# Kernel tuning notes

Measured on AMD Instinct MI355X. Metric: run time of the kernel, lower is better.

## Reference

```python
import jax, jax.numpy as jnp
import numpy as np

H, D = 8, 16
F = H * D              # hidden_dim = 128
L = 2                  # num HGT layers
NS = [50000, 20000, 10000]                     # gene, disease, drug node counts
EDGE_META = [(0, 0), (0, 1), (2, 0), (2, 1)]   # (src_type, dst_type) per edge type
ES = [300000, 150000, 100000, 50000]
OFFS = [0, NS[0], NS[0] + NS[1], NS[0] + NS[1] + NS[2]]
NTOT = OFFS[-1]
R, T = len(EDGE_META), len(NS)
SQRT_D = float(np.sqrt(D))


def setup_inputs() -> dict:
    key = jax.random.key(0)
    ks = jax.random.split(key, 32)
    inp = {}
    inp["x_gene"] = jax.random.normal(ks[0], (NS[0], F), jnp.float32)
    inp["x_disease"] = jax.random.normal(ks[1], (NS[1], F), jnp.float32)
    inp["x_drug"] = jax.random.normal(ks[2], (NS[2], F), jnp.float32)
    inp["Wkqv"] = 0.05 * jax.random.normal(ks[3], (L, T, F, 3 * F), jnp.float32)
    inp["bkqv"] = jnp.zeros((L, T, 3 * F), jnp.float32)
    inp["Ak"] = 0.1 * jax.random.normal(ks[4], (L, R, H, D, D), jnp.float32)
    inp["Av"] = 0.1 * jax.random.normal(ks[5], (L, R, H, D, D), jnp.float32)
    inp["prel"] = jnp.ones((L, R, H), jnp.float32)   # PyG inits p_rel to ones
    inp["Wout"] = 0.05 * jax.random.normal(ks[6], (L, T, F, F), jnp.float32)
    inp["bout"] = jnp.zeros((L, T, F), jnp.float32)
    inp["skip"] = jnp.ones((L, T), jnp.float32)      # PyG inits skip to 1
    names = ["ei_gg", "ei_gd", "ei_rg", "ei_rd"]
    for i, (name, (st, dt), E) in enumerate(zip(names, EDGE_META, ES)):
        src = jax.random.randint(ks[10 + 2 * i], (E,), 0, NS[st], dtype=jnp.int32)
        dst = jax.random.randint(ks[11 + 2 * i], (E,), 0, NS[dt], dtype=jnp.int32)
        inp[name] = jnp.stack([src, dst])
    return inp


def _hgt_layer(xs, eis, Wkqv_l, bkqv_l, Ak_l, Av_l, prel_l, Wout_l, bout_l, skip_l):
    """One PyG-style HGTConv layer over the heterogeneous graph."""
    kqv = [x @ Wkqv_l[t] + bkqv_l[t] for t, x in enumerate(xs)]
    k = [a[:, :F].reshape(-1, H, D) for a in kqv]
    q = [a[:, F:2 * F].reshape(-1, H, D) for a in kqv]
    v = [a[:, 2 * F:].reshape(-1, H, D) for a in kqv]

    alphas, dsts, ves = [], [], []
    for r, (st, dt) in enumerate(EDGE_META):
        src, dst = eis[r][0], eis[r][1]
        # relation-specific per-head transforms applied on source node set
        k_r = jnp.einsum('nhd,hde->nhe', k[st], Ak_l[r])
        v_r = jnp.einsum('nhd,hde->nhe', v[st], Av_l[r])
        ke = k_r[src]                      # [E, H, D]
        ve = v_r[src]                      # [E, H, D]
        qe = q[dt][dst]                    # [E, H, D]
        a = (qe * ke).sum(-1) * prel_l[r] / SQRT_D   # [E, H]
        alphas.append(a)
        dsts.append(dst + OFFS[dt])
        ves.append(ve)
    alpha = jnp.concatenate(alphas, 0)     # [Etot, H]
    dstg = jnp.concatenate(dsts, 0)        # [Etot]
    ve = jnp.concatenate(ves, 0)           # [Etot, H, D]

    # segment softmax over all incoming edges per destination node
    amax = jax.ops.segment_max(alpha, dstg, num_segments=NTOT)
    ex = jnp.exp(alpha - amax[dstg])
    denom = jax.ops.segment_sum(ex, dstg, num_segments=NTOT)
    w = ex / denom[dstg]
    out = jax.ops.segment_sum(ve * w[..., None], dstg, num_segments=NTOT)
    out = out.reshape(NTOT, F)

    new_xs = []
    for t, x in enumerate(xs):
        o_t = out[OFFS[t]:OFFS[t + 1]]
        o = jax.nn.gelu(o_t, approximate=False) @ Wout_l[t] + bout_l[t]
        a_s = jax.nn.sigmoid(skip_l[t])
        new_xs.append(a_s * o + (1.0 - a_s) * x)
    return new_xs


def reference(x_gene, x_disease, x_drug, Wkqv, bkqv, Ak, Av, prel, Wout, bout,
              skip, ei_gg, ei_gd, ei_rg, ei_rd):
    xs = [x_gene, x_disease, x_drug]
    eis = [ei_gg, ei_gd, ei_rg, ei_rd]
    for l in range(L):
        new = _hgt_layer(xs, eis, Wkqv[l], bkqv[l], Ak[l], Av[l], prel[l],
                         Wout[l], bout[l], skip[l])
        # encoder: dropout(relu(conv_out)) + residual; dropout = identity (eval)
        xs = [jax.nn.relu(n) + x for n, x in zip(new, xs)]
    return tuple(xs)
```

## Files before the change

kernel.cpp:

```cpp
#include <hip/hip_runtime.h>


#define NTOT  80000
#define ETOT  600000
#define NSRC  120000
#define SLOTS 128

typedef unsigned short u16;
typedef unsigned int   u32;
typedef __attribute__((ext_vector_type(8))) short short8;
typedef __attribute__((ext_vector_type(4))) float f32x4;

__device__ __forceinline__ float bf2f(u16 u){
  union { u32 i; float f; } v; v.i = ((u32)u) << 16; return v.f;
}
__device__ __forceinline__ u16 f2bf(float f){
  union { float f; u32 i; } v; v.f = f;
  u32 x = v.i;
  return (u16)((x + 0x7fffu + ((x >> 16) & 1u)) >> 16);
}
__device__ __forceinline__ void unp4(uint4 a, float* o){
  union { u32 i; float f; } t;
  t.i = a.x << 16;        o[0]=t.f;  t.i = a.x & 0xffff0000u; o[1]=t.f;
  t.i = a.y << 16;        o[2]=t.f;  t.i = a.y & 0xffff0000u; o[3]=t.f;
  t.i = a.z << 16;        o[4]=t.f;  t.i = a.z & 0xffff0000u; o[5]=t.f;
  t.i = a.w << 16;        o[6]=t.f;  t.i = a.w & 0xffff0000u; o[7]=t.f;
}
__device__ __forceinline__ void load16bf(const u16* p, float* o){
  unp4(*(const uint4*)p, o); unp4(*(const uint4*)(p + 8), o + 8);
}


#define PR0 2560000
#define PR1 (PR0 + NTOT)
#define PR2 (PR1 + 8*32768)
#define PR3 (PR2 + 2*6*16384)
#define PR4 (PR3 + 2048)

__global__ __launch_bounds__(256) void prep_all(
    const float* __restrict__ xg, const float* __restrict__ xd,
    const float* __restrict__ xr, float* __restrict__ X, u16* __restrict__ Xbf,
    int* __restrict__ cnt,
    const float* __restrict__ Wkqv, const float* __restrict__ bkqv,
    const float* __restrict__ Ak, const float* __restrict__ Av,
    const float* __restrict__ Wout,
    u16* __restrict__ WeffT, u16* __restrict__ WqT, u16* __restrict__ WoutT,
    float* __restrict__ beff)
{
  int i = blockIdx.x * 256 + threadIdx.x;
  if (i < PR0){
    const float* src; int off;
    if (i < 1600000)      { src = xg; off = i; }
    else if (i < 2240000) { src = xd; off = i - 1600000; }
    else                  { src = xr; off = i - 2240000; }
    float4 v = ((const float4*)src)[off];
    ((float4*)X)[i] = v;
    uint2 b;
    b.x = (u32)f2bf(v.x) | ((u32)f2bf(v.y) << 16);
    b.y = (u32)f2bf(v.z) | ((u32)f2bf(v.w) << 16);
    ((uint2*)Xbf)[i] = b;
    return;
  }
  if (i < PR1){ cnt[i - PR0] = 0; return; }
  if (i < PR2){
    int j = i - PR1;
    int lr = j >> 15, rem = j & 32767, n = rem >> 7, k = rem & 127;
    int l = lr >> 2, r = lr & 3;
    int st = (r >= 2) ? 2 : 0;
    const float* W = Wkqv + (size_t)(l*3 + st) * 49152;
    float acc = 0.f;
    if (n < 128){
      int h = n >> 4, e = n & 15;
      const float* Am = Ak + (size_t)(l*4 + r) * 2048 + h*256;
#pragma unroll
      for (int d = 0; d < 16; d++) acc += W[k*384 + h*16 + d] * Am[d*16 + e];
    } else {
      int n2 = n - 128, h = n2 >> 4, e = n2 & 15;
      const float* Am = Av + (size_t)(l*4 + r) * 2048 + h*256;
#pragma unroll
      for (int d = 0; d < 16; d++) acc += W[k*384 + 256 + h*16 + d] * Am[d*16 + e];
    }
    WeffT[j] = f2bf(acc);
    return;
  }
  if (i < PR3){
    int j = i - PR2;
    if (j < 6*16384){
      int lt = j >> 14, rem = j & 16383, n = rem >> 7, k = rem & 127;
      WqT[j] = f2bf(Wkqv[(size_t)lt*49152 + k*384 + 128 + n]);
    } else {
      int j2 = j - 6*16384;
      int lt = j2 >> 14, rem = j2 & 16383, n = rem >> 7, k = rem & 127;
      WoutT[j2] = f2bf(Wout[(size_t)lt*16384 + k*128 + n]);
    }
    return;
  }
  if (i < PR4){
    int m = i - PR3;
    int lr = m >> 8, jj = m & 255;
    int l = lr >> 2, r = lr & 3;
    int st = (r >= 2) ? 2 : 0;
    const float* b = bkqv + (size_t)(l*3 + st) * 384;
    float acc = 0.f;
    if (jj < 128){
      int h = jj >> 4, e = jj & 15;
      const float* Am = Ak + (size_t)(l*4 + r) * 2048 + h*256;
#pragma unroll
      for (int d = 0; d < 16; d++) acc += b[h*16 + d] * Am[d*16 + e];
    } else {
      int j2 = jj - 128, h = j2 >> 4, e = j2 & 15;
      const float* Am = Av + (size_t)(l*4 + r) * 2048 + h*256;
#pragma unroll
      for (int d = 0; d < 16; d++) acc += b[256 + h*16 + d] * Am[d*16 + e];
    }
    beff[lr * 256 + jj] = acc;
  }
}


__global__ __launch_bounds__(256) void scatter_direct(
    const int* __restrict__ e0, const int* __restrict__ e1,
    const int* __restrict__ e2, const int* __restrict__ e3,
    int* __restrict__ cnt, int* __restrict__ elist)
{
  int e = blockIdx.x * 256 + threadIdx.x;
  if (e >= ETOT) return;
  const int* ei; int E, loc, offd, rnoff, rel;
  if (e < 300000)      { ei = e0; E = 300000; loc = e;          offd = 0;     rnoff = 0;      rel = 0; }
  else if (e < 450000) { ei = e1; E = 150000; loc = e - 300000; offd = 50000; rnoff = 50000;  rel = 1; }
  else if (e < 550000) { ei = e2; E = 100000; loc = e - 450000; offd = 0;     rnoff = 100000; rel = 2; }
  else                 { ei = e3; E = 50000;  loc = e - 550000; offd = 50000; rnoff = 110000; rel = 3; }
  int src = ei[loc], dst = ei[E + loc];
  int dstg = offd + dst;
  int pos = atomicAdd(&cnt[dstg], 1);
  if (pos < SLOTS) elist[dstg*SLOTS + pos] = ((rnoff + src) << 2) | rel;
}


__device__ __forceinline__ void stage_bt(const u16* __restrict__ src, u16* BTl){
  int tid = threadIdx.x;
  const uint4* g = (const uint4*)src;
  uint4 tmp[8];
#pragma unroll
  for (int i = 0; i < 8; i++) tmp[i] = g[tid + i*256];
#pragma unroll
  for (int i = 0; i < 8; i++){
    int L = (tid + i*256) * 16;
    int Ls = L ^ (((L >> 8) & 7) << 4);
    *(uint4*)((char*)BTl + Ls) = tmp[i];
  }
  __syncthreads();
}

__device__ __forceinline__ void gemm_core16(
    const u16* __restrict__ A, const u16* BTl, int M, int bm,
    f32x4 acc[8])
{
  int tid = threadIdx.x;
  int lane = tid & 63, w = tid >> 6;
  int quad = lane >> 4, lm = lane & 15;
  int row = bm + w*16 + lm;
  short8 af[4];
  if (row < M){
    const u16* ap = A + (size_t)row*128 + quad*8;
#pragma unroll
    for (int c = 0; c < 4; c++) af[c] = *(const short8*)(ap + c*32);
  } else {
    short8 z = {0,0,0,0,0,0,0,0};
#pragma unroll
    for (int c = 0; c < 4; c++) af[c] = z;
  }
#pragma unroll
  for (int nt = 0; nt < 8; nt++) acc[nt] = (f32x4){0.f,0.f,0.f,0.f};
#pragma unroll
  for (int nt = 0; nt < 8; nt++){
    int rowb = nt*16 + lm;
    int base = rowb*256 + quad*16;
    int sw = (rowb & 7) << 4;
#pragma unroll
    for (int c = 0; c < 4; c++){
      short8 bf = *(const short8*)((const char*)BTl + ((base + c*64) ^ sw));
      acc[nt] = __builtin_amdgcn_mfma_f32_16x16x32_bf16(af[c], bf, acc[nt], 0, 0, 0);
    }
  }
}

__global__ __launch_bounds__(256) void mfma_gemm_qkv(
    const u16* __restrict__ Xbf,
    const u16* __restrict__ WqTl, const float* __restrict__ bl,
    const u16* __restrict__ WeffTl, const float* __restrict__ beffl,
    u16* __restrict__ qg, u16* __restrict__ kv)
{
  __shared__ u16 BTl[16384];
  int by = blockIdx.x;
  const u16* A; const u16* BT; const float* bias;
  u16* C; int ldc, bm, M, bn;
  if (by < 1252){
    int t, roff;
    if (by < 782)       { t = 0; bm = by*64;         M = 50000; roff = 0; }
    else if (by < 1095) { t = 1; bm = (by-782)*64;   M = 20000; roff = 50000; }
    else                { t = 2; bm = (by-1095)*64;  M = 10000; roff = 70000; }
    A = Xbf + (size_t)roff*128;
    BT = WqTl + (size_t)t*16384;
    bias = bl + (size_t)t*384 + 128;
    C = qg + (size_t)roff*128; ldc = 128; bn = 0;
  } else {
    int idx = by - 1252;
    bn = (idx < 1878) ? 0 : 128;
    int tile = (idx < 1878) ? idx : idx - 1878;
    int r, soff, ooff;
    if (tile < 782)       { r = 0; bm = tile*64;        M = 50000; soff = 0;     ooff = 0; }
    else if (tile < 1564) { r = 1; bm = (tile-782)*64;  M = 50000; soff = 0;     ooff = 50000; }
    else if (tile < 1721) { r = 2; bm = (tile-1564)*64; M = 10000; soff = 70000; ooff = 100000; }
    else                  { r = 3; bm = (tile-1721)*64; M = 10000; soff = 70000; ooff = 110000; }
    A = Xbf + (size_t)soff*128;
    BT = WeffTl + (size_t)r*32768 + (size_t)bn*128;
    bias = beffl + (size_t)r*256 + bn;
    C = kv + (size_t)ooff*256 + bn; ldc = 256;
  }
  stage_bt(BT, BTl);
  f32x4 acc[8];
  gemm_core16(A, BTl, M, bm, acc);
  int lane = threadIdx.x & 63, w = threadIdx.x >> 6;
  int quad = lane >> 4, lm = lane & 15;
#pragma unroll
  for (int nt = 0; nt < 8; nt++){
    int col = nt*16 + lm;
    float bb = bias[col];
#pragma unroll
    for (int i = 0; i < 4; i++){
      int r = bm + w*16 + quad*4 + i;
      if (r < M) C[(size_t)r*ldc + col] = f2bf(acc[nt][i] + bb);
    }
  }
}

__global__ __launch_bounds__(256) void mfma_gemm_out(
    const u16* __restrict__ Gall, const u16* __restrict__ WoutTl,
    const float* __restrict__ bl, const float* __restrict__ skipl,
    float* __restrict__ Xall, u16* __restrict__ Xbfall)
{
  __shared__ u16 BTl[16384];
  int by = blockIdx.x;
  int t, bm, M, roff;
  if (by < 782)       { t = 0; bm = by*64;         M = 50000; roff = 0; }
  else if (by < 1095) { t = 1; bm = (by-782)*64;   M = 20000; roff = 50000; }
  else                { t = 2; bm = (by-1095)*64;  M = 10000; roff = 70000; }
  stage_bt(WoutTl + (size_t)t*16384, BTl);
  const u16* A = Gall + (size_t)roff*128;
  const float* bias = bl + (size_t)t*128;
  float* X = Xall + (size_t)roff*128;
  u16* Xb = Xbfall ? (Xbfall + (size_t)roff*128) : (u16*)0;
  f32x4 acc[8];
  gemm_core16(A, BTl, M, bm, acc);
  float a_s = 1.f / (1.f + expf(-skipl[t]));
  float b_s = 1.f - a_s;
  int lane = threadIdx.x & 63, w = threadIdx.x >> 6;
  int quad = lane >> 4, lm = lane & 15;
#pragma unroll
  for (int nt = 0; nt < 8; nt++){
    int col = nt*16 + lm;
    float bb = bias[col];
#pragma unroll
    for (int i = 0; i < 4; i++){
      int r = bm + w*16 + quad*4 + i;
      if (r < M){
        float* xp = X + (size_t)r*128 + col;
        float x = *xp;
        float o = acc[nt][i] + bb;
        float xn = fmaxf(a_s*o + b_s*x, 0.f) + x;
        *xp = xn;
        if (Xb) Xb[(size_t)r*128 + col] = f2bf(xn);
      }
    }
  }
}


__global__ __launch_bounds__(256) void attn_kernel(
    u16* __restrict__ qg,
    const u16* __restrict__ kv,
    const float* __restrict__ prel,
    const int* __restrict__ cnt,
    const int* __restrict__ elist)
{
  int gid = blockIdx.x * 256 + threadIdx.x;
  int n = gid >> 4;
  if (n >= NTOT) return;
  int lane = threadIdx.x & 63;
  int sub = (lane >> 3) & 1;
  int h = lane & 7;
  float sc0 = prel[0*8+h]*0.25f, sc1 = prel[1*8+h]*0.25f,
        sc2 = prel[2*8+h]*0.25f, sc3 = prel[3*8+h]*0.25f;
  float q[16];
  load16bf(qg + (size_t)n * 128 + h*16, q);
  float acc[16] = {};
  float dsum = 0.f;
  int start = n * SLOTS, c = cnt[n];
  if (c > SLOTS) c = SLOTS;

  auto edge = [&](int ev, uint4 ka, uint4 kb, uint4 va, uint4 vb){
    float ke[16], ve[16];
    unp4(ka, ke); unp4(kb, ke + 8);
    unp4(va, ve); unp4(vb, ve + 8);
    float a = 0.f;
#pragma unroll
    for (int d = 0; d < 16; d++) a += q[d] * ke[d];
    int r = ev & 3;
    float s = (r == 0) ? sc0 : (r == 1) ? sc1 : (r == 2) ? sc2 : sc3;
    float ex = expf(a * s);
    dsum += ex;
#pragma unroll
    for (int d = 0; d < 16; d++) acc[d] += ex * ve[d];
  };

  int idx = sub;
#pragma unroll 1
  for (; idx + 6 < c; idx += 8){
    int e0 = elist[start + idx + 0], e1 = elist[start + idx + 2],
        e2 = elist[start + idx + 4], e3 = elist[start + idx + 6];
    const u16* p0 = kv + (size_t)(e0 >> 2) * 256 + h*16;
    const u16* p1 = kv + (size_t)(e1 >> 2) * 256 + h*16;
    const u16* p2 = kv + (size_t)(e2 >> 2) * 256 + h*16;
    const u16* p3 = kv + (size_t)(e3 >> 2) * 256 + h*16;
    uint4 k0a = *(const uint4*)p0,         k0b = *(const uint4*)(p0 + 8);
    uint4 k1a = *(const uint4*)p1,         k1b = *(const uint4*)(p1 + 8);
    uint4 k2a = *(const uint4*)p2,         k2b = *(const uint4*)(p2 + 8);
    uint4 k3a = *(const uint4*)p3,         k3b = *(const uint4*)(p3 + 8);
    uint4 v0a = *(const uint4*)(p0 + 128), v0b = *(const uint4*)(p0 + 136);
    uint4 v1a = *(const uint4*)(p1 + 128), v1b = *(const uint4*)(p1 + 136);
    uint4 v2a = *(const uint4*)(p2 + 128), v2b = *(const uint4*)(p2 + 136);
    uint4 v3a = *(const uint4*)(p3 + 128), v3b = *(const uint4*)(p3 + 136);
    edge(e0, k0a, k0b, v0a, v0b);
    edge(e1, k1a, k1b, v1a, v1b);
    edge(e2, k2a, k2b, v2a, v2b);
    edge(e3, k3a, k3b, v3a, v3b);
  }
#pragma unroll 1
  for (; idx < c; idx += 2){
    int ev = elist[start + idx];
    const u16* p = kv + (size_t)(ev >> 2) * 256 + h*16;
    uint4 ka = *(const uint4*)p,         kb = *(const uint4*)(p + 8);
    uint4 va = *(const uint4*)(p + 128), vb = *(const uint4*)(p + 136);
    edge(ev, ka, kb, va, vb);
  }

  dsum += __shfl_xor(dsum, 8);
#pragma unroll
  for (int d = 0; d < 16; d++) acc[d] += __shfl_xor(acc[d], 8);

  if (sub == 0){
    float inv = (c > 0) ? 1.f / dsum : 0.f;
    u16 o[16];
#pragma unroll
    for (int d = 0; d < 16; d++){
      float x = acc[d] * inv;
      o[d] = f2bf(0.5f * x * (1.f + erff(x * 0.70710678118654752f)));
    }
    uint4 p0, p1;
    p0.x = o[0]|(o[1]<<16);   p0.y = o[2]|(o[3]<<16);
    p0.z = o[4]|(o[5]<<16);   p0.w = o[6]|(o[7]<<16);
    p1.x = o[8]|(o[9]<<16);   p1.y = o[10]|(o[11]<<16);
    p1.z = o[12]|(o[13]<<16); p1.w = o[14]|(o[15]<<16);
    u16* op = qg + (size_t)n * 128 + h*16;
    *(uint4*)op = p0; *(uint4*)(op + 8) = p1;
  }
}


extern "C" void kernel_launch(void* const* d_in, const int* in_sizes, int n_in,
                              void* d_out, int out_size, void* d_ws, size_t ws_size,
                              hipStream_t stream)
{
  const float* xg   = (const float*)d_in[0];
  const float* xd   = (const float*)d_in[1];
  const float* xr_  = (const float*)d_in[2];
  const float* Wkqv = (const float*)d_in[3];
  const float* bkqv = (const float*)d_in[4];
  const float* Ak   = (const float*)d_in[5];
  const float* Av   = (const float*)d_in[6];
  const float* prel = (const float*)d_in[7];
  const float* Wout = (const float*)d_in[8];
  const float* bout = (const float*)d_in[9];
  const float* skip = (const float*)d_in[10];
  const int* ei[4] = {(const int*)d_in[11], (const int*)d_in[12],
                      (const int*)d_in[13], (const int*)d_in[14]};

  float* X = (float*)d_out;

  char* p = (char*)d_ws;
  auto alloc = [&](size_t b)->void*{ void* r = (void*)p; p += (b + 255) & ~(size_t)255; return r; };
  int*   cnt   = (int*)  alloc((size_t)NTOT * 4);
  int*   elist = (int*)  alloc((size_t)NTOT * SLOTS * 4);
  float* beff  = (float*)alloc((size_t)8 * 256 * 4);
  u16*   qg    = (u16*)  alloc((size_t)NTOT * 128 * 2);
  u16*   kv    = (u16*)  alloc((size_t)NSRC * 256 * 2);
  u16*   Xbf   = (u16*)  alloc((size_t)NTOT * 128 * 2);
  u16*   WqT   = (u16*)  alloc((size_t)6 * 16384 * 2);
  u16*   WeffT = (u16*)  alloc((size_t)8 * 32768 * 2);
  u16*   WoutT = (u16*)  alloc((size_t)6 * 16384 * 2);
  (void)ws_size; (void)in_sizes; (void)n_in; (void)out_size;

  prep_all<<<(PR4 + 255)/256, 256, 0, stream>>>(
      xg, xd, xr_, X, Xbf, cnt,
      Wkqv, bkqv, Ak, Av, Wout, WeffT, WqT, WoutT, beff);

  scatter_direct<<<(ETOT+255)/256, 256, 0, stream>>>(
      ei[0], ei[1], ei[2], ei[3], cnt, elist);

  for (int l = 0; l < 2; l++){
    mfma_gemm_qkv<<<1252 + 3756, 256, 0, stream>>>(
        Xbf,
        WqT + (size_t)l*3*16384, bkqv + (size_t)l*3*384,
        WeffT + (size_t)l*4*32768, beff + (size_t)l*4*256,
        qg, kv);
    attn_kernel<<<5000, 256, 0, stream>>>(qg, kv, prel + l*32, cnt, elist);
    mfma_gemm_out<<<1252, 256, 0, stream>>>(
        qg, WoutT + (size_t)l*3*16384, bout + (size_t)l*3*128, skip + l*3,
        X, (l == 0) ? Xbf : (u16*)0);
  }
}
```

Measured before the change: 420.9 us.

## Fuse attention with output projection and merge edge scatter into prep kernel

The attention kernel now keeps each 16-node tile's GELU output in shared memory and immediately runs the Wout MFMA projection plus the skip and residual epilogue, replacing the separate output GEMM and the bf16 round trip through global memory. Edge scattering is folded into the prep kernel, and the count reset moves to a memset. This removes two launches and the intermediate global traffic, but each attention block must now stage the full 32KB Wout tile into LDS, which adds per-block load and lowers occupancy. Folding the scatter into prep also relies on the memset finishing before the kernel starts, which stream ordering guarantees.

```diff
diff --git a/kernel.cpp b/kernel.cpp
--- a/kernel.cpp
+++ b/kernel.cpp
@@ -11,9 +11,6 @@
 typedef __attribute__((ext_vector_type(8))) short short8;
 typedef __attribute__((ext_vector_type(4))) float f32x4;
 
-__device__ __forceinline__ float bf2f(u16 u){
-  union { u32 i; float f; } v; v.i = ((u32)u) << 16; return v.f;
-}
 __device__ __forceinline__ u16 f2bf(float f){
   union { float f; u32 i; } v; v.f = f;
   u32 x = v.i;
@@ -32,20 +29,22 @@
 
 
 #define PR0 2560000
-#define PR1 (PR0 + NTOT)
-#define PR2 (PR1 + 8*32768)
-#define PR3 (PR2 + 2*6*16384)
-#define PR4 (PR3 + 2048)
+#define PR1 (PR0 + 8*32768)
+#define PR2 (PR1 + 2*6*16384)
+#define PR3 (PR2 + 2048)
+#define PR4 (PR3 + ETOT)
 
 __global__ __launch_bounds__(256) void prep_all(
     const float* __restrict__ xg, const float* __restrict__ xd,
     const float* __restrict__ xr, float* __restrict__ X, u16* __restrict__ Xbf,
-    int* __restrict__ cnt,
     const float* __restrict__ Wkqv, const float* __restrict__ bkqv,
     const float* __restrict__ Ak, const float* __restrict__ Av,
     const float* __restrict__ Wout,
     u16* __restrict__ WeffT, u16* __restrict__ WqT, u16* __restrict__ WoutT,
-    float* __restrict__ beff)
+    float* __restrict__ beff,
+    const int* __restrict__ e0, const int* __restrict__ e1,
+    const int* __restrict__ e2, const int* __restrict__ e3,
+    int* __restrict__ cnt, int* __restrict__ elist)
 {
   int i = blockIdx.x * 256 + threadIdx.x;
   if (i < PR0){
@@ -61,9 +60,8 @@
     ((uint2*)Xbf)[i] = b;
     return;
   }
-  if (i < PR1){ cnt[i - PR0] = 0; return; }
-  if (i < PR2){
-    int j = i - PR1;
+  if (i < PR1){
+    int j = i - PR0;
     int lr = j >> 15, rem = j & 32767, n = rem >> 7, k = rem & 127;
     int l = lr >> 2, r = lr & 3;
     int st = (r >= 2) ? 2 : 0;
@@ -83,8 +81,8 @@
     WeffT[j] = f2bf(acc);
     return;
   }
-  if (i < PR3){
-    int j = i - PR2;
+  if (i < PR2){
+    int j = i - PR1;
     if (j < 6*16384){
       int lt = j >> 14, rem = j & 16383, n = rem >> 7, k = rem & 127;
       WqT[j] = f2bf(Wkqv[(size_t)lt*49152 + k*384 + 128 + n]);
@@ -95,8 +93,8 @@
     }
     return;
   }
-  if (i < PR4){
-    int m = i - PR3;
+  if (i < PR3){
+    int m = i - PR2;
     int lr = m >> 8, jj = m & 255;
     int l = lr >> 2, r = lr & 3;
     int st = (r >= 2) ? 2 : 0;
@@ -114,26 +112,20 @@
       for (int d = 0; d < 16; d++) acc += b[256 + h*16 + d] * Am[d*16 + e];
     }
     beff[lr * 256 + jj] = acc;
-  }
-}
-
-
-__global__ __launch_bounds__(256) void scatter_direct(
-    const int* __restrict__ e0, const int* __restrict__ e1,
-    const int* __restrict__ e2, const int* __restrict__ e3,
-    int* __restrict__ cnt, int* __restrict__ elist)
-{
-  int e = blockIdx.x * 256 + threadIdx.x;
-  if (e >= ETOT) return;
-  const int* ei; int E, loc, offd, rnoff, rel;
-  if (e < 300000)      { ei = e0; E = 300000; loc = e;          offd = 0;     rnoff = 0;      rel = 0; }
-  else if (e < 450000) { ei = e1; E = 150000; loc = e - 300000; offd = 50000; rnoff = 50000;  rel = 1; }
-  else if (e < 550000) { ei = e2; E = 100000; loc = e - 450000; offd = 0;     rnoff = 100000; rel = 2; }
-  else                 { ei = e3; E = 50000;  loc = e - 550000; offd = 50000; rnoff = 110000; rel = 3; }
-  int src = ei[loc], dst = ei[E + loc];
-  int dstg = offd + dst;
-  int pos = atomicAdd(&cnt[dstg], 1);
-  if (pos < SLOTS) elist[dstg*SLOTS + pos] = ((rnoff + src) << 2) | rel;
+    return;
+  }
+  if (i < PR4){
+    int e = i - PR3;
+    const int* ei; int E, loc, offd, rnoff, rel;
+    if (e < 300000)      { ei = e0; E = 300000; loc = e;          offd = 0;     rnoff = 0;      rel = 0; }
+    else if (e < 450000) { ei = e1; E = 150000; loc = e - 300000; offd = 50000; rnoff = 50000;  rel = 1; }
+    else if (e < 550000) { ei = e2; E = 100000; loc = e - 450000; offd = 0;     rnoff = 100000; rel = 2; }
+    else                 { ei = e3; E = 50000;  loc = e - 550000; offd = 50000; rnoff = 110000; rel = 3; }
+    int src = ei[loc], dst = ei[E + loc];
+    int dstg = offd + dst;
+    int pos = atomicAdd(&cnt[dstg], 1);
+    if (pos < SLOTS) elist[dstg*SLOTS + pos] = ((rnoff + src) << 2) | rel;
+  }
 }
 
 
@@ -149,7 +141,6 @@
     int Ls = L ^ (((L >> 8) & 7) << 4);
     *(uint4*)((char*)BTl + Ls) = tmp[i];
   }
-  __syncthreads();
 }
 
 __device__ __forceinline__ void gemm_core16(
@@ -219,6 +210,7 @@
     C = kv + (size_t)ooff*256 + bn; ldc = 256;
   }
   stage_bt(BT, BTl);
+  __syncthreads();
   f32x4 acc[8];
   gemm_core16(A, BTl, M, bm, acc);
   int lane = threadIdx.x & 63, w = threadIdx.x >> 6;
@@ -235,59 +227,32 @@
   }
 }
 
-__global__ __launch_bounds__(256) void mfma_gemm_out(
-    const u16* __restrict__ Gall, const u16* __restrict__ WoutTl,
-    const float* __restrict__ bl, const float* __restrict__ skipl,
-    float* __restrict__ Xall, u16* __restrict__ Xbfall)
-{
-  __shared__ u16 BTl[16384];
-  int by = blockIdx.x;
-  int t, bm, M, roff;
-  if (by < 782)       { t = 0; bm = by*64;         M = 50000; roff = 0; }
-  else if (by < 1095) { t = 1; bm = (by-782)*64;   M = 20000; roff = 50000; }
-  else                { t = 2; bm = (by-1095)*64;  M = 10000; roff = 70000; }
-  stage_bt(WoutTl + (size_t)t*16384, BTl);
-  const u16* A = Gall + (size_t)roff*128;
-  const float* bias = bl + (size_t)t*128;
-  float* X = Xall + (size_t)roff*128;
-  u16* Xb = Xbfall ? (Xbfall + (size_t)roff*128) : (u16*)0;
-  f32x4 acc[8];
-  gemm_core16(A, BTl, M, bm, acc);
-  float a_s = 1.f / (1.f + expf(-skipl[t]));
-  float b_s = 1.f - a_s;
-  int lane = threadIdx.x & 63, w = threadIdx.x >> 6;
-  int quad = lane >> 4, lm = lane & 15;
-#pragma unroll
-  for (int nt = 0; nt < 8; nt++){
-    int col = nt*16 + lm;
-    float bb = bias[col];
-#pragma unroll
-    for (int i = 0; i < 4; i++){
-      int r = bm + w*16 + quad*4 + i;
-      if (r < M){
-        float* xp = X + (size_t)r*128 + col;
-        float x = *xp;
-        float o = acc[nt][i] + bb;
-        float xn = fmaxf(a_s*o + b_s*x, 0.f) + x;
-        *xp = xn;
-        if (Xb) Xb[(size_t)r*128 + col] = f2bf(xn);
-      }
-    }
-  }
-}
-
-
-__global__ __launch_bounds__(256) void attn_kernel(
-    u16* __restrict__ qg,
+
+__global__ __launch_bounds__(256) void attn_out(
+    const u16* __restrict__ qg,
     const u16* __restrict__ kv,
     const float* __restrict__ prel,
     const int* __restrict__ cnt,
-    const int* __restrict__ elist)
+    const int* __restrict__ elist,
+    const u16* __restrict__ WoutTl,
+    const float* __restrict__ bl,
+    const float* __restrict__ skipl,
+    float* __restrict__ Xall, u16* __restrict__ Xbfall)
 {
-  int gid = blockIdx.x * 256 + threadIdx.x;
-  int n = gid >> 4;
-  if (n >= NTOT) return;
-  int lane = threadIdx.x & 63;
+  __shared__ u16 BT[16384];
+  __shared__ u16 G[2048];
+  int bid = blockIdx.x;
+  int t, bm, roff;
+  if (bid < 3125)      { t = 0; bm = bid*16;        roff = 0; }
+  else if (bid < 4375) { t = 1; bm = (bid-3125)*16; roff = 50000; }
+  else                 { t = 2; bm = (bid-4375)*16; roff = 70000; }
+
+  stage_bt(WoutTl + (size_t)t*16384, BT);
+
+  int tid = threadIdx.x;
+  int slot = tid >> 4;
+  int n = roff + bm + slot;
+  int lane = tid & 63;
   int sub = (lane >> 3) & 1;
   int h = lane & 7;
   float sc0 = prel[0*8+h]*0.25f, sc1 = prel[1*8+h]*0.25f,
@@ -362,8 +327,55 @@
     p0.z = o[4]|(o[5]<<16);   p0.w = o[6]|(o[7]<<16);
     p1.x = o[8]|(o[9]<<16);   p1.y = o[10]|(o[11]<<16);
     p1.z = o[12]|(o[13]<<16); p1.w = o[14]|(o[15]<<16);
-    u16* op = qg + (size_t)n * 128 + h*16;
-    *(uint4*)op = p0; *(uint4*)(op + 8) = p1;
+    int b0 = slot*256 + h*32;
+    int sw = (slot & 7) << 4;
+    *(uint4*)((char*)G + (b0 ^ sw))        = p0;
+    *(uint4*)((char*)G + ((b0 + 16) ^ sw)) = p1;
+  }
+  __syncthreads();
+
+  int w = tid >> 6;
+  int quad = lane >> 4, lm = lane & 15;
+  short8 af[4];
+  {
+    int base = lm*256 + quad*16;
+    int sw = (lm & 7) << 4;
+#pragma unroll
+    for (int c2 = 0; c2 < 4; c2++)
+      af[c2] = *(const short8*)((const char*)G + ((base + c2*64) ^ sw));
+  }
+  f32x4 oacc[2];
+#pragma unroll
+  for (int nt = 0; nt < 2; nt++){
+    oacc[nt] = (f32x4){0.f,0.f,0.f,0.f};
+    int rowb = w*32 + nt*16 + lm;
+    int base = rowb*256 + quad*16;
+    int sw = (rowb & 7) << 4;
+#pragma unroll
+    for (int c2 = 0; c2 < 4; c2++){
+      short8 bf = *(const short8*)((const char*)BT + ((base + c2*64) ^ sw));
+      oacc[nt] = __builtin_amdgcn_mfma_f32_16x16x32_bf16(af[c2], bf, oacc[nt], 0, 0, 0);
+    }
+  }
+  float a_s = 1.f / (1.f + expf(-skipl[t]));
+  float b_s = 1.f - a_s;
+  const float* bias = bl + (size_t)t*128;
+  float* X = Xall + (size_t)roff*128;
+  u16* Xb = Xbfall ? (Xbfall + (size_t)roff*128) : (u16*)0;
+#pragma unroll
+  for (int nt = 0; nt < 2; nt++){
+    int col = w*32 + nt*16 + lm;
+    float bb = bias[col];
+#pragma unroll
+    for (int i = 0; i < 4; i++){
+      int r = bm + quad*4 + i;
+      float* xp = X + (size_t)r*128 + col;
+      float x = *xp;
+      float o = oacc[nt][i] + bb;
+      float xn = fmaxf(a_s*o + b_s*x, 0.f) + x;
+      *xp = xn;
+      if (Xb) Xb[(size_t)r*128 + col] = f2bf(xn);
+    }
   }
 }
 
@@ -401,11 +413,11 @@
   u16*   WoutT = (u16*)  alloc((size_t)6 * 16384 * 2);
   (void)ws_size; (void)in_sizes; (void)n_in; (void)out_size;
 
+  hipMemsetAsync(cnt, 0, (size_t)NTOT * 4, stream);
+
   prep_all<<<(PR4 + 255)/256, 256, 0, stream>>>(
-      xg, xd, xr_, X, Xbf, cnt,
-      Wkqv, bkqv, Ak, Av, Wout, WeffT, WqT, WoutT, beff);
-
-  scatter_direct<<<(ETOT+255)/256, 256, 0, stream>>>(
+      xg, xd, xr_, X, Xbf,
+      Wkqv, bkqv, Ak, Av, Wout, WeffT, WqT, WoutT, beff,
       ei[0], ei[1], ei[2], ei[3], cnt, elist);
 
   for (int l = 0; l < 2; l++){
@@ -414,9 +426,9 @@
         WqT + (size_t)l*3*16384, bkqv + (size_t)l*3*384,
         WeffT + (size_t)l*4*32768, beff + (size_t)l*4*256,
         qg, kv);
-    attn_kernel<<<5000, 256, 0, stream>>>(qg, kv, prel + l*32, cnt, elist);
-    mfma_gemm_out<<<1252, 256, 0, stream>>>(
-        qg, WoutT + (size_t)l*3*16384, bout + (size_t)l*3*128, skip + l*3,
+    attn_out<<<5000, 256, 0, stream>>>(
+        qg, kv, prel + l*32, cnt, elist,
+        WoutT + (size_t)l*3*16384, bout + (size_t)l*3*128, skip + l*3,
         X, (l == 0) ? Xbf : (u16*)0);
   }
 }
```

New measurement: 409.6 us. 1.03x faster.
